# Optimization experiments

Hardware: AMD Instinct MI355X
Metric: run time of the kernel (lower is better)

## Reference

```python
import jax, jax.numpy as jnp
import numpy as np

# torch_dtype_to_gain is an undefined global in the original source; we interpret
# it as the standard sqrt(d_k) attention gain for the input dtype.

def reference(qk, qk_scaling_factor, query, key, value):
    D = query.shape[-1]
    gain = jnp.sqrt(jnp.asarray(D, dtype=query.dtype))
    # scores: [B, Sq, Sk]
    scores = jnp.einsum('bqd,bkd->bqk', query, key)
    scores = scores / gain
    scores = scores / qk_scaling_factor  # broadcast [1,1]
    # p=0.0, is_training=False -> dropout is identity
    o = jnp.einsum('bqk,bkv->bqv', scores, value)  # [B, Sq, Dv]
    return o


def setup_inputs() -> dict:
    key0 = jax.random.key(0)
    k1, k2, k3, k4 = jax.random.split(key0, 4)
    B, Sq, Sk, D, Dv = 8, 2048, 2048, 128, 128
    return {
        'qk': jnp.ones((1, 1), dtype=jnp.float32),  # overwritten in forward; dummy
        'qk_scaling_factor': jnp.ones((1, 1), dtype=jnp.float32),
        'query': jax.random.normal(k1, (B, Sq, D), dtype=jnp.float32),
        'key': jax.random.normal(k2, (B, Sk, D), dtype=jnp.float32),
        'value': jax.random.normal(k3, (B, Sk, Dv), dtype=jnp.float32),
    }
```

## Files before the change

### kernel.cpp

```cpp
#include <hip/hip_runtime.h>


#define BATCH 8
#define SEQ 2048
#define DIM 128

typedef __attribute__((ext_vector_type(8))) short short8;
typedef __attribute__((ext_vector_type(4))) float f32x4;

__device__ __forceinline__ unsigned int f2bf(float f) {
    unsigned int u = __float_as_uint(f);
    u += 0x7fffu + ((u >> 16) & 1u);
    return u >> 16;
}

__global__ __launch_bounds__(256) void vtk_atomic(const float* __restrict__ K,
                                                  const float* __restrict__ V,
                                                  float* __restrict__ T) {
    __shared__ float Vc[64 * 128];
    __shared__ float Kc[64 * 64];
    const int blk = blockIdx.x;
    const int b   = blk >> 6;
    const int kc  = (blk >> 1) & 31;
    const int dh  = blk & 1;
    const int tid = threadIdx.x;

    const float* Vg = V + ((size_t)b * SEQ + kc * 64) * DIM;
    const float* Kg = K + ((size_t)b * SEQ + kc * 64) * DIM + dh * 64;

    #pragma unroll
    for (int i = 0; i < 8; i++) {
        int idx = tid + i * 256;
        ((float4*)Vc)[idx] = ((const float4*)Vg)[idx];
    }
    #pragma unroll
    for (int i = 0; i < 4; i++) {
        int idx = tid + i * 256;
        int r = idx >> 4, c = idx & 15;
        ((float4*)Kc)[idx] = *(const float4*)(Kg + r * DIM + c * 4);
    }
    __syncthreads();

    const int td = tid & 15;
    const int te = tid >> 4;

    float acc[8][4];
    #pragma unroll
    for (int i = 0; i < 8; i++)
        #pragma unroll
        for (int j = 0; j < 4; j++) acc[i][j] = 0.0f;

    for (int k = 0; k < 64; k++) {
        const float4 kd = *(const float4*)&Kc[k * 64 + td * 4];
        const float4 va = *(const float4*)&Vc[k * 128 + te * 8];
        const float4 vb = *(const float4*)&Vc[k * 128 + te * 8 + 4];
        const float ve[8] = {va.x, va.y, va.z, va.w, vb.x, vb.y, vb.z, vb.w};
        const float kv[4] = {kd.x, kd.y, kd.z, kd.w};
        #pragma unroll
        for (int i = 0; i < 8; i++)
            #pragma unroll
            for (int j = 0; j < 4; j++)
                acc[i][j] = fmaf(ve[i], kv[j], acc[i][j]);
    }

    __syncthreads();

    #pragma unroll
    for (int i = 0; i < 8; i++) {
        float4 w = {acc[i][0], acc[i][1], acc[i][2], acc[i][3]};
        *(float4*)&Vc[(te * 8 + i) * 64 + td * 4] = w;
    }
    __syncthreads();

    float* Tb = T + (size_t)b * (DIM * DIM) + dh * 64;
    #pragma unroll
    for (int i = 0; i < 32; i++) {
        int u  = i * 256 + tid;
        int e  = u >> 6;
        int dl = u & 63;
        atomicAdd(&Tb[e * DIM + dl], Vc[u]);
    }
}

__global__ __launch_bounds__(256) void qt_f32t(const float* __restrict__ Q,
                                               const float* __restrict__ T,
                                               const float* __restrict__ qk_sf,
                                               float* __restrict__ O) {
    __shared__ unsigned short Ts[128 * 136];
    __shared__ unsigned short Qs[32 * 136];
    const int b   = blockIdx.x >> 6;
    const int q0  = (blockIdx.x & 63) * 32;
    const int tid = threadIdx.x;

    const float s = 1.0f / (sqrtf(128.0f) * qk_sf[0]);

    const float4* Tg = (const float4*)(T + (size_t)b * (DIM * DIM));
    #pragma unroll
    for (int i = 0; i < 16; i++) {
        int idx = tid + i * 256;
        int row = idx >> 5, c = idx & 31;
        float4 v = Tg[idx];
        uint2 w;
        w.x = f2bf(v.x) | (f2bf(v.y) << 16);
        w.y = f2bf(v.z) | (f2bf(v.w) << 16);
        *(uint2*)&Ts[row * 136 + c * 4] = w;
    }
    const float4* Qg = (const float4*)(Q + ((size_t)b * SEQ + q0) * DIM);
    #pragma unroll
    for (int i = 0; i < 4; i++) {
        int idx = tid + i * 256;
        int row = idx >> 5, c = idx & 31;
        float4 v = Qg[idx];
        uint2 w;
        w.x = f2bf(v.x * s) | (f2bf(v.y * s) << 16);
        w.y = f2bf(v.z * s) | (f2bf(v.w * s) << 16);
        *(uint2*)&Qs[row * 136 + c * 4] = w;
    }
    __syncthreads();

    const int wave = tid >> 6, lane = tid & 63;
    const int lm   = lane & 15, quad = lane >> 4;
    const int mrow = (wave & 1) * 16;
    const int n0   = (wave >> 1) * 64;

    f32x4 acc[4] = {{0,0,0,0},{0,0,0,0},{0,0,0,0},{0,0,0,0}};
    #pragma unroll
    for (int ks = 0; ks < 4; ks++) {
        short8 a = *(const short8*)&Qs[(mrow + lm) * 136 + ks * 32 + quad * 8];
        #pragma unroll
        for (int nt = 0; nt < 4; nt++) {
            short8 bb = *(const short8*)&Ts[(n0 + nt * 16 + lm) * 136 + ks * 32 + quad * 8];
            acc[nt] = __builtin_amdgcn_mfma_f32_16x16x32_bf16(a, bb, acc[nt], 0, 0, 0);
        }
    }

    float* Og = O + ((size_t)b * SEQ + q0) * DIM;
    #pragma unroll
    for (int nt = 0; nt < 4; nt++)
        #pragma unroll
        for (int r = 0; r < 4; r++) {
            const int row = mrow + quad * 4 + r;
            const int col = n0 + nt * 16 + lm;
            Og[row * DIM + col] = acc[nt][r];
        }
}

extern "C" void kernel_launch(void* const* d_in, const int* in_sizes, int n_in,
                              void* d_out, int out_size, void* d_ws, size_t ws_size,
                              hipStream_t stream) {
    const float* qk_sf = (const float*)d_in[1];
    const float* Q = (const float*)d_in[2];
    const float* K = (const float*)d_in[3];
    const float* V = (const float*)d_in[4];
    float* O = (float*)d_out;

    float* T = (float*)d_ws;

    hipMemsetAsync(T, 0, (size_t)BATCH * DIM * DIM * sizeof(float), stream);
    vtk_atomic<<<dim3(512), dim3(256), 0, stream>>>(K, V, T);
    qt_f32t<<<dim3(BATCH * 64), dim3(256), 0, stream>>>(Q, T, qk_sf, O);
}
```

Measured before the change: 104.9 us.

## Replace atomic accumulation with bf16 partials plus separate reduction kernel

The V^T K partial products are no longer summed with float atomics into a zeroed fp32 buffer. Each block now writes its 64x64 partial as bf16 to a workspace, a new reduce kernel sums the 32 chunks, applies the scale, and writes a bf16 transposed T. The final MFMA kernel then loads bf16 T directly without conversion. This drops the memset and the atomic contention but adds a kernel launch, and rounding each partial to bf16 before summing loses precision.

Result: faster. 94.49 us (-9.9%).

```diff
diff --git a/kernel.cpp b/kernel.cpp
--- a/kernel.cpp
+++ b/kernel.cpp
@@ -14,9 +14,9 @@
     return u >> 16;
 }
 
-__global__ __launch_bounds__(256) void vtk_atomic(const float* __restrict__ K,
-                                                  const float* __restrict__ V,
-                                                  float* __restrict__ T) {
+__global__ __launch_bounds__(256) void vtk_partial(const float* __restrict__ K,
+                                                   const float* __restrict__ V,
+                                                   unsigned short* __restrict__ P) {
     __shared__ float Vc[64 * 128];
     __shared__ float Kc[64 * 64];
     const int blk = blockIdx.x;
@@ -44,47 +44,60 @@
     const int td = tid & 15;
     const int te = tid >> 4;
 
-    float acc[8][4];
+    f32x4 acc[8];
     #pragma unroll
-    for (int i = 0; i < 8; i++)
-        #pragma unroll
-        for (int j = 0; j < 4; j++) acc[i][j] = 0.0f;
+    for (int i = 0; i < 8; i++) acc[i] = (f32x4){0.f, 0.f, 0.f, 0.f};
 
     for (int k = 0; k < 64; k++) {
-        const float4 kd = *(const float4*)&Kc[k * 64 + td * 4];
+        const f32x4 kd = *(const f32x4*)&Kc[k * 64 + td * 4];
         const float4 va = *(const float4*)&Vc[k * 128 + te * 8];
         const float4 vb = *(const float4*)&Vc[k * 128 + te * 8 + 4];
         const float ve[8] = {va.x, va.y, va.z, va.w, vb.x, vb.y, vb.z, vb.w};
-        const float kv[4] = {kd.x, kd.y, kd.z, kd.w};
         #pragma unroll
         for (int i = 0; i < 8; i++)
-            #pragma unroll
-            for (int j = 0; j < 4; j++)
-                acc[i][j] = fmaf(ve[i], kv[j], acc[i][j]);
+            acc[i] += kd * ve[i];
     }
 
-    __syncthreads();
-
+    unsigned short* Pb = P + (size_t)blk * 8192;
     #pragma unroll
     for (int i = 0; i < 8; i++) {
-        float4 w = {acc[i][0], acc[i][1], acc[i][2], acc[i][3]};
-        *(float4*)&Vc[(te * 8 + i) * 64 + td * 4] = w;
-    }
-    __syncthreads();
-
-    float* Tb = T + (size_t)b * (DIM * DIM) + dh * 64;
-    #pragma unroll
-    for (int i = 0; i < 32; i++) {
-        int u  = i * 256 + tid;
-        int e  = u >> 6;
-        int dl = u & 63;
-        atomicAdd(&Tb[e * DIM + dl], Vc[u]);
+        uint2 w;
+        w.x = f2bf(acc[i][0]) | (f2bf(acc[i][1]) << 16);
+        w.y = f2bf(acc[i][2]) | (f2bf(acc[i][3]) << 16);
+        *(uint2*)(Pb + (te * 8 + i) * 64 + td * 4) = w;
     }
 }
 
-__global__ __launch_bounds__(256) void qt_f32t(const float* __restrict__ Q,
-                                               const float* __restrict__ T,
-                                               const float* __restrict__ qk_sf,
+__global__ __launch_bounds__(256) void reduce_t(const unsigned short* __restrict__ P,
+                                                const float* __restrict__ qk_sf,
+                                                unsigned short* __restrict__ Tt) {
+    const int u   = blockIdx.x * 256 + threadIdx.x;
+    const int b   = u >> 12;
+    const int rem = u & 4095;
+    const int e   = rem >> 5;
+    const int d0  = (rem & 31) * 4;
+    const int dh  = d0 >> 6;
+    const int dl  = d0 & 63;
+
+    const unsigned short* Pb = P + ((size_t)(b * 64 + dh) * 8192) + e * 64 + dl;
+    float a0 = 0.f, a1 = 0.f, a2 = 0.f, a3 = 0.f;
+    #pragma unroll 8
+    for (int kc = 0; kc < 32; kc++) {
+        uint2 w = *(const uint2*)(Pb + (size_t)kc * 16384);
+        a0 += __uint_as_float(w.x << 16);
+        a1 += __uint_as_float(w.x & 0xffff0000u);
+        a2 += __uint_as_float(w.y << 16);
+        a3 += __uint_as_float(w.y & 0xffff0000u);
+    }
+    const float s = 1.0f / (sqrtf(128.0f) * qk_sf[0]);
+    uint2 o;
+    o.x = f2bf(a0 * s) | (f2bf(a1 * s) << 16);
+    o.y = f2bf(a2 * s) | (f2bf(a3 * s) << 16);
+    *(uint2*)(Tt + (size_t)b * 16384 + e * 128 + d0) = o;
+}
+
+__global__ __launch_bounds__(256) void qt_mfma(const float* __restrict__ Q,
+                                               const unsigned short* __restrict__ Tt,
                                                float* __restrict__ O) {
     __shared__ unsigned short Ts[128 * 136];
     __shared__ unsigned short Qs[32 * 136];
@@ -92,18 +105,12 @@
     const int q0  = (blockIdx.x & 63) * 32;
     const int tid = threadIdx.x;
 
-    const float s = 1.0f / (sqrtf(128.0f) * qk_sf[0]);
-
-    const float4* Tg = (const float4*)(T + (size_t)b * (DIM * DIM));
+    const uint4* Tg = (const uint4*)(Tt + (size_t)b * 16384);
     #pragma unroll
-    for (int i = 0; i < 16; i++) {
+    for (int i = 0; i < 8; i++) {
         int idx = tid + i * 256;
-        int row = idx >> 5, c = idx & 31;
-        float4 v = Tg[idx];
-        uint2 w;
-        w.x = f2bf(v.x) | (f2bf(v.y) << 16);
-        w.y = f2bf(v.z) | (f2bf(v.w) << 16);
-        *(uint2*)&Ts[row * 136 + c * 4] = w;
+        int row = idx >> 4, c = idx & 15;
+        *(uint4*)&Ts[row * 136 + c * 8] = Tg[idx];
     }
     const float4* Qg = (const float4*)(Q + ((size_t)b * SEQ + q0) * DIM);
     #pragma unroll
@@ -112,8 +119,8 @@
         int row = idx >> 5, c = idx & 31;
         float4 v = Qg[idx];
         uint2 w;
-        w.x = f2bf(v.x * s) | (f2bf(v.y * s) << 16);
-        w.y = f2bf(v.z * s) | (f2bf(v.w * s) << 16);
+        w.x = f2bf(v.x) | (f2bf(v.y) << 16);
+        w.y = f2bf(v.z) | (f2bf(v.w) << 16);
         *(uint2*)&Qs[row * 136 + c * 4] = w;
     }
     __syncthreads();
@@ -154,9 +161,10 @@
     const float* V = (const float*)d_in[4];
     float* O = (float*)d_out;
 
-    float* T = (float*)d_ws;
+    unsigned short* P  = (unsigned short*)d_ws;
+    unsigned short* Tt = (unsigned short*)((char*)d_ws + (size_t)512 * 8192 * 2);
 
-    hipMemsetAsync(T, 0, (size_t)BATCH * DIM * DIM * sizeof(float), stream);
-    vtk_atomic<<<dim3(512), dim3(256), 0, stream>>>(K, V, T);
-    qt_f32t<<<dim3(BATCH * 64), dim3(256), 0, stream>>>(Q, T, qk_sf, O);
+    vtk_partial<<<dim3(512), dim3(256), 0, stream>>>(K, V, P);
+    reduce_t<<<dim3(128), dim3(256), 0, stream>>>(P, qk_sf, Tt);
+    qt_mfma<<<dim3(BATCH * 64), dim3(256), 0, stream>>>(Q, Tt, O);
 }
```
